# Performance work log

Hardware: AMD Instinct MI355X
Metric: run time of the kernel (lower is better)

Reference implementation:

```python
import jax, jax.numpy as jnp
import numpy as np

B = 1024        # batch of clips
MAX_LEN = 14    # temporal length, pinned by spatial_shapes=[[max_len,1]]
D_MODEL = 1024
N_HEADS = 16
N_POINTS = 4
H_SP, W_SP = MAX_LEN, 1  # level-0 spatial shape (H, W)


def setup_inputs() -> dict:
    key = jax.random.key(0)
    ks = jax.random.split(key, 12)
    s = 0.02
    lin = lambda k, i, o: (jax.random.normal(k, (i, o), jnp.float32) * s)
    vec = lambda k, o: (jax.random.normal(k, (o,), jnp.float32) * s)
    return {
        "x": jax.random.normal(ks[0], (B, MAX_LEN, D_MODEL), jnp.float32),
        "W_value": lin(ks[1], D_MODEL, D_MODEL), "b_value": vec(ks[2], D_MODEL),
        "W_off": lin(ks[3], D_MODEL, N_HEADS * N_POINTS * 2), "b_off": vec(ks[4], N_HEADS * N_POINTS * 2),
        "W_attn": lin(ks[5], D_MODEL, N_HEADS * N_POINTS), "b_attn": vec(ks[6], N_HEADS * N_POINTS),
        "W_out": lin(ks[7], D_MODEL, D_MODEL), "b_out": vec(ks[8], D_MODEL),
        "W_proj": lin(ks[9], D_MODEL, D_MODEL), "b_proj": vec(ks[10], D_MODEL),
    }


def _msdeform(x, W_value, b_value, W_off, b_off, W_attn, b_attn, W_out, b_out):
    Bq, T, D = x.shape
    heads, P = N_HEADS, N_POINTS
    hd = D // heads
    # value projection -> [B, heads, N=H*W, hd]
    value = (x @ W_value + b_value).reshape(Bq, T, heads, hd).transpose(0, 2, 1, 3)
    # sampling offsets [B,T,heads,P,2] and softmax attention weights [B,T,heads,P]
    off = (x @ W_off + b_off).reshape(Bq, T, heads, P, 2)
    aw = jax.nn.softmax((x @ W_attn + b_attn).reshape(Bq, T, heads, P), axis=-1)
    # reference points: x-coord = linspace(0,1,T), y-coord = 0
    ref = jnp.linspace(0.0, 1.0, T, dtype=x.dtype)
    ref_pts = jnp.stack([ref, jnp.zeros_like(ref)], axis=-1)  # [T,2]
    norm = jnp.array([W_SP, H_SP], dtype=x.dtype)  # offset_normalizer = (W, H)
    locs = ref_pts[None, :, None, None, :] + off / norm  # [B,T,heads,P,2] in [0,1] coords
    # grid_sample bilinear, align_corners=False, padding_mode='zeros':
    # pixel coord = loc * size - 0.5
    ix = locs[..., 0] * W_SP - 0.5
    iy = locs[..., 1] * H_SP - 0.5
    x0 = jnp.floor(ix); y0 = jnp.floor(iy)
    fx = ix - x0; fy = iy - y0
    x0i = x0.astype(jnp.int32); y0i = y0.astype(jnp.int32)
    out = jnp.zeros((Bq, heads, T * P, hd), x.dtype)
    corners = ((0, 0, (1 - fx) * (1 - fy)), (1, 0, fx * (1 - fy)),
               (0, 1, (1 - fx) * fy), (1, 1, fx * fy))
    for dx, dy, w in corners:
        xx = x0i + dx; yy = y0i + dy
        valid = ((xx >= 0) & (xx < W_SP) & (yy >= 0) & (yy < H_SP)).astype(x.dtype)
        idx = jnp.clip(yy, 0, H_SP - 1) * W_SP + jnp.clip(xx, 0, W_SP - 1)  # [B,T,heads,P]
        idx_t = idx.transpose(0, 2, 1, 3).reshape(Bq, heads, T * P)
        v = jnp.take_along_axis(value, idx_t[..., None], axis=2)  # [B,heads,T*P,hd]
        wt = (w * valid).transpose(0, 2, 1, 3).reshape(Bq, heads, T * P)
        out = out + v * wt[..., None]
    out = out.reshape(Bq, heads, T, P, hd)
    attn = jnp.einsum('bhqpd,bqhp->bqhd', out, aw).reshape(Bq, T, D)
    return attn @ W_out + b_out


def reference(x, W_value, b_value, W_off, b_off, W_attn, b_attn, W_out, b_out, W_proj, b_proj):
    y = _msdeform(x, W_value, b_value, W_off, b_off, W_attn, b_attn, W_out, b_out)
    return y @ W_proj + b_proj
```

## Files before the change

kernel.cpp:

```cpp
#include <hip/hip_runtime.h>
#include <hip/hip_bf16.h>

using bf16 = __hip_bfloat16;
typedef __attribute__((ext_vector_type(8))) short bf16x8;
typedef __attribute__((ext_vector_type(4))) float f32x4;

#define NB   1024
#define TT   14
#define DM   1024
#define ROWS (NB*TT)
#define NCAT 1280

__device__ __forceinline__ unsigned short f2b(float f) {
  union { bf16 h; unsigned short u; } cv; cv.h = __float2bfloat16(f); return cv.u;
}

__device__ __forceinline__ void gload16(const bf16* g, bf16* l) {
  __builtin_amdgcn_global_load_lds((const __attribute__((address_space(1))) void*)g,
                                   (__attribute__((address_space(3))) void*)l, 16, 0, 0);
}

__global__ __launch_bounds__(256) void k_prep_all(
    const float* __restrict__ x_in,
    const float* __restrict__ Wv, const float* __restrict__ Wo,
    const float* __restrict__ Wa, const float* __restrict__ Wproj,
    const float* __restrict__ Wout,
    const float* __restrict__ bv, const float* __restrict__ bo,
    const float* __restrict__ ba, const float* __restrict__ b_out,
    const float* __restrict__ b_proj,
    bf16* __restrict__ x_bf,
    bf16* __restrict__ wcat_t, bf16* __restrict__ wproj_t,
    bf16* __restrict__ wout_b, float* __restrict__ bcat,
    float* __restrict__ bcomb) {
  __shared__ float t[32][33];
  const int x = blockIdx.x, y = blockIdx.y;
  const int lx = threadIdx.x & 31, ly = threadIdx.x >> 5;
  if (y < 72) {
    const float* src; bf16* dst; int base, width;
    if (y < 40) {
      dst = wcat_t;
      int n0 = y * 32;
      if (n0 < 1024)      { src = Wv; base = 0;    width = 1024; }
      else if (n0 < 1152) { src = Wo; base = 1024; width = 128;  }
      else if (n0 < 1216) { src = Wa; base = 1152; width = 64;   }
      else                { src = nullptr; base = 0; width = 1;  }
      int k0 = x * 32, n0b = n0;
#pragma unroll
      for (int r = 0; r < 32; r += 8)
        t[ly + r][lx] = src ? src[(size_t)(k0 + ly + r) * width + (n0b - base + lx)] : 0.0f;
      __syncthreads();
#pragma unroll
      for (int r = 0; r < 32; r += 8)
        dst[(size_t)(n0b + ly + r) * 1024 + (k0 + lx)] = __float2bfloat16(t[lx][ly + r]);
    } else {
      int n0 = (y - 40) * 32, k0 = x * 32;
#pragma unroll
      for (int r = 0; r < 32; r += 8)
        t[ly + r][lx] = Wproj[(size_t)(k0 + ly + r) * 1024 + (n0 + lx)];
      __syncthreads();
#pragma unroll
      for (int r = 0; r < 32; r += 8)
        wproj_t[(size_t)(n0 + ly + r) * 1024 + (k0 + lx)] = __float2bfloat16(t[lx][ly + r]);
    }
  } else if (y < 80) {
    int i0 = ((y - 72) * 32 + x) * 1024 + threadIdx.x;
#pragma unroll
    for (int r = 0; r < 4; ++r) {
      int i = i0 + r * 256;
      float4 v = reinterpret_cast<const float4*>(Wout)[i];
      ushort4 o;
      o.x = f2b(v.x); o.y = f2b(v.y); o.z = f2b(v.z); o.w = f2b(v.w);
      reinterpret_cast<ushort4*>(wout_b)[i] = o;
    }
  } else if (y == 80) {
    if (x < 5) {
      int i = x * 256 + threadIdx.x;
      if (i < NCAT) {
        float v = 0.0f;
        if (i < 1024) v = bv[i];
        else if (i < 1152) v = bo[i - 1024];
        else if (i < 1216) v = ba[i - 1152];
        bcat[i] = v;
      }
    } else if (x < 21) {
      __shared__ float part[4][64];
      int j0 = (x - 5) * 64;
      int jl = threadIdx.x & 63, ip = threadIdx.x >> 6;
      int j = j0 + jl;
      float acc = 0.0f;
      int i0 = ip * 256;
      for (int i = i0; i < i0 + 256; ++i)
        acc = fmaf(b_out[i], Wproj[(size_t)i * 1024 + j], acc);
      part[ip][jl] = acc;
      __syncthreads();
      if (threadIdx.x < 64) {
        int jj = j0 + threadIdx.x;
        bcomb[jj] = part[0][threadIdx.x] + part[1][threadIdx.x] +
                    part[2][threadIdx.x] + part[3][threadIdx.x] + b_proj[jj];
      }
    }
  } else {
    int id = (y - 81) * 32 + x;
    int i0 = id * 2048 + threadIdx.x;
#pragma unroll
    for (int r = 0; r < 8; ++r) {
      int i = i0 + r * 256;
      float4 v = reinterpret_cast<const float4*>(x_in)[i];
      ushort4 o;
      o.x = f2b(v.x); o.y = f2b(v.y); o.z = f2b(v.z); o.w = f2b(v.w);
      reinterpret_cast<ushort4*>(x_bf)[i] = o;
    }
  }
}

template<int OUT1, int OUT2>
__global__ __launch_bounds__(512, 4) void k_gemm2(
    const bf16* __restrict__ A1, const bf16* __restrict__ B1,
    void* __restrict__ C1v, const float* __restrict__ bias1,
    int N1, int K1, int lda1, int ldb1, int nx1, int nwg1,
    const bf16* __restrict__ A2, const bf16* __restrict__ B2,
    void* __restrict__ C2v, const float* __restrict__ bias2,
    int N2, int K2, int lda2, int ldb2, int nx2) {
  __shared__ bf16 As[3 * 8192];
  __shared__ bf16 Bs[3 * 4096];

  const int tid = threadIdx.x, w = tid >> 6, l = tid & 63;
  const int wm = w >> 1, wn = w & 1;

  const bf16 *A, *Bt; void* Cv; const float* bias;
  int N, K, lda, ldb, bx, by; bool ob;
  if ((int)blockIdx.x < nwg1) {
    int bid = blockIdx.x;
    int q = nwg1 >> 3, r = nwg1 & 7;
    int xcd = bid & 7, li = bid >> 3;
    bid = (xcd < r ? xcd * (q + 1) : r * (q + 1) + (xcd - r) * q) + li;
    A = A1; Bt = B1; Cv = C1v; bias = bias1;
    N = N1; K = K1; lda = lda1; ldb = ldb1;
    bx = bid % nx1; by = bid / nx1; ob = (OUT1 != 0);
  } else {
    int bid = blockIdx.x - nwg1;
    A = A2; Bt = B2; Cv = C2v; bias = bias2;
    N = N2; K = K2; lda = lda2; ldb = ldb2;
    bx = bid % nx2; by = bid / nx2; ob = (OUT2 != 0);
  }
  const int row0 = by * 256, col0 = bx * 128;
  f32x4 acc[4][4] = {};

  const int sr = tid >> 2;
  const int sc = ((tid & 3) ^ (sr & 3)) * 8;
  const bf16* Ab0 = A  + (size_t)(row0 + sr) * lda + sc;
  const bf16* Ab1 = Ab0 + (size_t)128 * lda;
  const bf16* Bb  = Bt + (size_t)(col0 + sr) * ldb + sc;

  const int fr = l & 15, g = l >> 4;
  const int fs = (g ^ (fr & 3)) * 8;
  int aoff[4], boff[4];
#pragma unroll
  for (int i = 0; i < 4; ++i) {
    aoff[i] = (wm * 64 + i * 16 + fr) * 32 + fs;
    boff[i] = (wn * 64 + i * 16 + fr) * 32 + fs;
  }

  auto STAGE = [&](int s, int kt) {
    const int ko = kt * 32;
    gload16(Ab0 + ko, As + s * 8192 + tid * 8);
    gload16(Ab1 + ko, As + s * 8192 + 4096 + tid * 8);
    gload16(Bb  + ko, Bs + s * 4096 + tid * 8);
  };
  auto COMPUTE = [&](int s) {
    const bf16* as = As + s * 8192;
    const bf16* bs = Bs + s * 4096;
    bf16x8 af[4], bfm[4];
#pragma unroll
    for (int i = 0; i < 4; ++i) af[i]  = *(const bf16x8*)(as + aoff[i]);
#pragma unroll
    for (int i = 0; i < 4; ++i) bfm[i] = *(const bf16x8*)(bs + boff[i]);
    __builtin_amdgcn_s_setprio(1);
#pragma unroll
    for (int mi = 0; mi < 4; ++mi)
#pragma unroll
      for (int ni = 0; ni < 4; ++ni)
        acc[mi][ni] = __builtin_amdgcn_mfma_f32_16x16x32_bf16(bfm[ni], af[mi], acc[mi][ni], 0, 0, 0);
    __builtin_amdgcn_s_setprio(0);
  };

  const int nk = K >> 5;
  STAGE(0, 0);
  STAGE(1, 1);
  int cur = 0;
  for (int t = 0; t < nk; ++t) {
    if (t < nk - 1) asm volatile("s_waitcnt vmcnt(3)" ::: "memory");
    else            asm volatile("s_waitcnt vmcnt(0)" ::: "memory");
    __builtin_amdgcn_s_barrier();
    asm volatile("" ::: "memory");
    if (t + 2 < nk) {
      int s2 = cur + 2; if (s2 >= 3) s2 -= 3;
      STAGE(s2, t + 2);
    }
    COMPUTE(cur);
    if (++cur == 3) cur = 0;
  }

#pragma unroll
  for (int mi = 0; mi < 4; ++mi) {
    int gr = row0 + wm * 64 + mi * 16 + fr;
#pragma unroll
    for (int ni = 0; ni < 4; ++ni) {
      int gc = col0 + wn * 64 + ni * 16 + g * 4;
      float b0 = 0, b1 = 0, b2 = 0, b3 = 0;
      if (bias) {
        float4 bv = *reinterpret_cast<const float4*>(bias + gc);
        b0 = bv.x; b1 = bv.y; b2 = bv.z; b3 = bv.w;
      }
      float v0 = acc[mi][ni][0] + b0, v1 = acc[mi][ni][1] + b1;
      float v2 = acc[mi][ni][2] + b2, v3 = acc[mi][ni][3] + b3;
      if (ob) {
        ushort4 u; u.x = f2b(v0); u.y = f2b(v1); u.z = f2b(v2); u.w = f2b(v3);
        *reinterpret_cast<ushort4*>((bf16*)Cv + (size_t)gr * N + gc) = u;
      } else {
        float4 o; o.x = v0; o.y = v1; o.z = v2; o.w = v3;
        *reinterpret_cast<float4*>((float*)Cv + (size_t)gr * N + gc) = o;
      }
    }
  }
}

__global__ __launch_bounds__(256) void k_sample(const bf16* __restrict__ C1,
                                                bf16* __restrict__ y) {
  const int wave = threadIdx.x >> 6, lane = threadIdx.x & 63;
  const int row = blockIdx.x * 4 + wave;
  const int b = row / TT, t = row - b * TT;
  const bf16* r1 = C1 + (size_t)row * NCAT;

  float offx, offy;
  {
    ushort2 u = *reinterpret_cast<const ushort2*>(r1 + 1024 + lane * 2);
    offx = __uint_as_float(((unsigned)u.x) << 16);
    offy = __uint_as_float(((unsigned)u.y) << 16);
  }
  float logit;
  {
    unsigned short u = reinterpret_cast<const unsigned short*>(r1)[1152 + lane];
    logit = __uint_as_float(((unsigned)u) << 16);
  }
  float m = fmaxf(logit, __shfl_xor(logit, 1));
  m = fmaxf(m, __shfl_xor(m, 2));
  float e = __expf(logit - m);
  float s = e + __shfl_xor(e, 1);
  s = s + __shfl_xor(s, 2);
  float aw = e / s;

  const float refx = (float)t * (1.0f / 13.0f);
  float ix = refx + offx - 0.5f;
  float xf = floorf(ix);
  float fx = ix - xf;
  float wx = (xf == 0.0f) ? (1.0f - fx) : ((xf == -1.0f) ? fx : 0.0f);

  float iy = offy - 0.5f;
  float yf = floorf(iy);
  float fy = iy - yf;
  int y0 = (int)yf, y1 = y0 + 1;
  float w0 = (y0 >= 0 && y0 < TT) ? (1.0f - fy) : 0.0f;
  float w1 = (y1 >= 0 && y1 < TT) ? fy : 0.0f;
  int i0 = max(0, min(TT - 1, y0));
  int i1 = max(0, min(TT - 1, y1));
  float cw0 = aw * wx * w0;
  float cw1 = aw * wx * w1;

  const bf16* vb = C1 + (size_t)(b * TT) * NCAT;
  float acc[16];
#pragma unroll
  for (int h = 0; h < 16; ++h) acc[h] = 0.0f;
#pragma unroll
  for (int j = 0; j < 64; ++j) {
    float c0 = __shfl(cw0, j);
    float c1 = __shfl(cw1, j);
    int a0 = __shfl(i0, j);
    int a1 = __shfl(i1, j);
    const int hh = j >> 2;
    float v0 = __bfloat162float(vb[(size_t)a0 * NCAT + hh * 64 + lane]);
    float v1 = __bfloat162float(vb[(size_t)a1 * NCAT + hh * 64 + lane]);
    acc[hh] = fmaf(c0, v0, fmaf(c1, v1, acc[hh]));
  }
#pragma unroll
  for (int h = 0; h < 16; ++h)
    y[(size_t)row * DM + h * 64 + lane] = __float2bfloat16(acc[h]);
}

extern "C" void kernel_launch(void* const* d_in, const int* in_sizes, int n_in,
                              void* d_out, int out_size, void* d_ws, size_t ws_size,
                              hipStream_t stream) {
  (void)in_sizes; (void)n_in; (void)out_size; (void)ws_size;
  const float* x       = (const float*)d_in[0];
  const float* W_value = (const float*)d_in[1];
  const float* b_value = (const float*)d_in[2];
  const float* W_off   = (const float*)d_in[3];
  const float* b_off   = (const float*)d_in[4];
  const float* W_attn  = (const float*)d_in[5];
  const float* b_attn  = (const float*)d_in[6];
  const float* W_out   = (const float*)d_in[7];
  const float* b_out   = (const float*)d_in[8];
  const float* W_proj  = (const float*)d_in[9];
  const float* b_proj  = (const float*)d_in[10];

  char* ws = (char*)d_ws;
  bf16*  x_bf    = (bf16*)(ws);
  bf16*  y_bf    = x_bf;
  bf16*  C1      = (bf16*)(ws + 29360128);
  bf16*  Wcat_t  = (bf16*)(ws + 66060288);
  float* bcat    = (float*)(ws + 68681728);
  bf16*  Wout_b  = (bf16*)(ws + 68686848);
  bf16*  Wproj_t = (bf16*)(ws + 70784000);
  bf16*  Wc_t    = (bf16*)(ws + 72881152);
  float* bcomb   = (float*)(ws + 74978304);

  k_prep_all<<<dim3(32, 137), 256, 0, stream>>>(
      x, W_value, W_off, W_attn, W_proj, W_out,
      b_value, b_off, b_attn, b_out, b_proj,
      x_bf, Wcat_t, Wproj_t, Wout_b, bcat, bcomb);

  k_gemm2<1, 1><<<560 + 32, 512, 0, stream>>>(
      x_bf, Wcat_t, C1, bcat, NCAT, DM, DM, DM, NCAT / 128, 560,
      Wproj_t, Wout_b, Wc_t, nullptr, 1024, 1024, 1024, 1024, 8);

  k_sample<<<ROWS / 4, 256, 0, stream>>>(C1, y_bf);

  k_gemm2<0, 0><<<448, 512, 0, stream>>>(
      y_bf, Wc_t, (float*)d_out, bcomb, DM, DM, DM, DM, DM / 128, 448,
      y_bf, Wc_t, (float*)d_out, bcomb, DM, DM, DM, DM, DM / 128);
}
```

Measured before the change: 176.6 us.

## Switch GEMMs to 256x256 tiles with 8-phase double-buffered K=64 pipeline

Replaces the 256x128-tile, 3-stage GEMM with a 256x256 tile per workgroup. Each of the 8 waves now computes 128x64, and the K step is 64, split into four half-phases that interleave LDS fragment reads, asynchronous global-to-LDS staging and barriers. Larger tiles raise arithmetic intensity and reduce operand reloads. The trade-off is half as many workgroups (296 and 224 on 256 CUs), occupancy of one block per CU, more barriers per K step, and removal of the LDS XOR swizzle, which may cause bank conflicts.

Result: slower. 188.8 us (+6.9%).

```diff
diff --git a/kernel.cpp b/kernel.cpp
--- a/kernel.cpp
+++ b/kernel.cpp
@@ -114,18 +114,17 @@
 }
 
 template<int OUT1, int OUT2>
-__global__ __launch_bounds__(512, 4) void k_gemm2(
+__global__ __launch_bounds__(512, 1) void k_gemm8p(
     const bf16* __restrict__ A1, const bf16* __restrict__ B1,
     void* __restrict__ C1v, const float* __restrict__ bias1,
     int N1, int K1, int lda1, int ldb1, int nx1, int nwg1,
     const bf16* __restrict__ A2, const bf16* __restrict__ B2,
     void* __restrict__ C2v, const float* __restrict__ bias2,
     int N2, int K2, int lda2, int ldb2, int nx2) {
-  __shared__ bf16 As[3 * 8192];
-  __shared__ bf16 Bs[3 * 4096];
-
+  __shared__ bf16 As[2][2][8192];
+  __shared__ bf16 Bs[2][2][8192];
   const int tid = threadIdx.x, w = tid >> 6, l = tid & 63;
-  const int wm = w >> 1, wn = w & 1;
+  const int wm = w >> 2, wn = w & 3;
 
   const bf16 *A, *Bt; void* Cv; const float* bias;
   int N, K, lda, ldb, bx, by; bool ob;
@@ -143,67 +142,67 @@
     N = N2; K = K2; lda = lda2; ldb = ldb2;
     bx = bid % nx2; by = bid / nx2; ob = (OUT2 != 0);
   }
-  const int row0 = by * 256, col0 = bx * 128;
-  f32x4 acc[4][4] = {};
-
-  const int sr = tid >> 2;
-  const int sc = ((tid & 3) ^ (sr & 3)) * 8;
-  const bf16* Ab0 = A  + (size_t)(row0 + sr) * lda + sc;
-  const bf16* Ab1 = Ab0 + (size_t)128 * lda;
-  const bf16* Bb  = Bt + (size_t)(col0 + sr) * ldb + sc;
+  const int row0 = by * 256, col0 = bx * 256;
+
+  const int srow = tid >> 2, sslot = (tid & 3) * 8;
+  const bf16* Ag = A  + (size_t)(row0 + srow) * lda + sslot;
+  const bf16* Bg = Bt + (size_t)(col0 + srow) * ldb + sslot;
+
+#define SA(dd, kh, t) { const int ko = (t) * 64 + (kh) * 32;                    \
+    gload16(Ag + ko,                     &As[dd][kh][srow * 32 + sslot]);       \
+    gload16(Ag + (size_t)128 * lda + ko, &As[dd][kh][(128 + srow) * 32 + sslot]); }
+#define SB(dd, kh, t) { const int ko = (t) * 64 + (kh) * 32;                    \
+    gload16(Bg + ko,                     &Bs[dd][kh][srow * 32 + sslot]);       \
+    gload16(Bg + (size_t)128 * ldb + ko, &Bs[dd][kh][(128 + srow) * 32 + sslot]); }
 
   const int fr = l & 15, g = l >> 4;
-  const int fs = (g ^ (fr & 3)) * 8;
-  int aoff[4], boff[4];
-#pragma unroll
-  for (int i = 0; i < 4; ++i) {
-    aoff[i] = (wm * 64 + i * 16 + fr) * 32 + fs;
-    boff[i] = (wn * 64 + i * 16 + fr) * 32 + fs;
-  }
-
-  auto STAGE = [&](int s, int kt) {
-    const int ko = kt * 32;
-    gload16(Ab0 + ko, As + s * 8192 + tid * 8);
-    gload16(Ab1 + ko, As + s * 8192 + 4096 + tid * 8);
-    gload16(Bb  + ko, Bs + s * 4096 + tid * 8);
-  };
-  auto COMPUTE = [&](int s) {
-    const bf16* as = As + s * 8192;
-    const bf16* bs = Bs + s * 4096;
-    bf16x8 af[4], bfm[4];
-#pragma unroll
-    for (int i = 0; i < 4; ++i) af[i]  = *(const bf16x8*)(as + aoff[i]);
-#pragma unroll
-    for (int i = 0; i < 4; ++i) bfm[i] = *(const bf16x8*)(bs + boff[i]);
-    __builtin_amdgcn_s_setprio(1);
-#pragma unroll
-    for (int mi = 0; mi < 4; ++mi)
-#pragma unroll
-      for (int ni = 0; ni < 4; ++ni)
-        acc[mi][ni] = __builtin_amdgcn_mfma_f32_16x16x32_bf16(bfm[ni], af[mi], acc[mi][ni], 0, 0, 0);
-    __builtin_amdgcn_s_setprio(0);
-  };
-
-  const int nk = K >> 5;
-  STAGE(0, 0);
-  STAGE(1, 1);
-  int cur = 0;
-  for (int t = 0; t < nk; ++t) {
-    if (t < nk - 1) asm volatile("s_waitcnt vmcnt(3)" ::: "memory");
-    else            asm volatile("s_waitcnt vmcnt(0)" ::: "memory");
-    __builtin_amdgcn_s_barrier();
-    asm volatile("" ::: "memory");
-    if (t + 2 < nk) {
-      int s2 = cur + 2; if (s2 >= 3) s2 -= 3;
-      STAGE(s2, t + 2);
-    }
-    COMPUTE(cur);
-    if (++cur == 3) cur = 0;
-  }
-
-#pragma unroll
-  for (int mi = 0; mi < 4; ++mi) {
-    int gr = row0 + wm * 64 + mi * 16 + fr;
+  f32x4 acc[8][4] = {};
+
+  const int nt = K >> 6;
+  SB(0, 0, 0) SA(0, 0, 0) SB(0, 1, 0) SA(0, 1, 0)
+  if (nt > 1) { SB(1, 0, 1) SA(1, 0, 1) SB(1, 1, 1) }
+  asm volatile("s_waitcnt vmcnt(10)" ::: "memory");
+  __builtin_amdgcn_s_barrier();
+  asm volatile("" ::: "memory");
+
+  for (int t = 0; t < nt; ++t) {
+    const int d = t & 1;
+    bf16x8 bfm[4];
+
+#define PH(kh, fh, STAGE_STMT, VMWAIT_STMT)                                      \
+    {                                                                            \
+      bf16x8 af[4];                                                              \
+      _Pragma("unroll") for (int i = 0; i < 4; ++i)                              \
+        af[i] = *(const bf16x8*)&As[d][kh][(wm * 128 + (fh) * 64 + i * 16 + fr) * 32 + g * 8]; \
+      if ((fh) == 0) {                                                           \
+        _Pragma("unroll") for (int i = 0; i < 4; ++i)                            \
+          bfm[i] = *(const bf16x8*)&Bs[d][kh][(wn * 64 + i * 16 + fr) * 32 + g * 8]; \
+      }                                                                          \
+      STAGE_STMT;                                                                \
+      VMWAIT_STMT;                                                               \
+      __builtin_amdgcn_s_barrier();                                              \
+      __builtin_amdgcn_s_setprio(1);                                             \
+      _Pragma("unroll") for (int i = 0; i < 4; ++i)                              \
+        _Pragma("unroll") for (int n = 0; n < 4; ++n)                            \
+          acc[(fh) * 4 + i][n] = __builtin_amdgcn_mfma_f32_16x16x32_bf16(        \
+              bfm[n], af[i], acc[(fh) * 4 + i][n], 0, 0, 0);                     \
+      __builtin_amdgcn_s_setprio(0);                                             \
+      __builtin_amdgcn_s_barrier();                                              \
+      asm volatile("" ::: "memory");                                             \
+    }
+
+    PH(0, 0, { if (t + 1 < nt) SA(d ^ 1, 1, t + 1) }, { })
+    PH(0, 1, { if (t + 2 < nt) SB(d, 0, t + 2) },
+       { if (t < nt - 1) { asm volatile("s_waitcnt vmcnt(4)" ::: "memory"); }
+         else            { asm volatile("s_waitcnt vmcnt(0)" ::: "memory"); } })
+    PH(1, 0, { if (t + 2 < nt) SA(d, 0, t + 2) }, { })
+    PH(1, 1, { if (t + 2 < nt) SB(d, 1, t + 2) }, { })
+#undef PH
+  }
+
+#pragma unroll
+  for (int mi = 0; mi < 8; ++mi) {
+    int gr = row0 + wm * 128 + (mi >> 2) * 64 + (mi & 3) * 16 + fr;
 #pragma unroll
     for (int ni = 0; ni < 4; ++ni) {
       int gc = col0 + wn * 64 + ni * 16 + g * 4;
@@ -223,6 +222,8 @@
       }
     }
   }
+#undef SA
+#undef SB
 }
 
 __global__ __launch_bounds__(256) void k_sample(const bf16* __restrict__ C1,
@@ -319,13 +320,13 @@
       b_value, b_off, b_attn, b_out, b_proj,
       x_bf, Wcat_t, Wproj_t, Wout_b, bcat, bcomb);
 
-  k_gemm2<1, 1><<<560 + 32, 512, 0, stream>>>(
-      x_bf, Wcat_t, C1, bcat, NCAT, DM, DM, DM, NCAT / 128, 560,
-      Wproj_t, Wout_b, Wc_t, nullptr, 1024, 1024, 1024, 1024, 8);
+  k_gemm8p<1, 1><<<280 + 16, 512, 0, stream>>>(
+      x_bf, Wcat_t, C1, bcat, NCAT, DM, DM, DM, 5, 280,
+      Wproj_t, Wout_b, Wc_t, nullptr, 1024, 1024, 1024, 1024, 4);
 
   k_sample<<<ROWS / 4, 256, 0, stream>>>(C1, y_bf);
 
-  k_gemm2<0, 0><<<448, 512, 0, stream>>>(
-      y_bf, Wc_t, (float*)d_out, bcomb, DM, DM, DM, DM, DM / 128, 448,
-      y_bf, Wc_t, (float*)d_out, bcomb, DM, DM, DM, DM, DM / 128);
-}
+  k_gemm8p<0, 0><<<224, 512, 0, stream>>>(
+      y_bf, Wc_t, (float*)d_out, bcomb, DM, DM, DM, DM, 4, 224,
+      y_bf, Wc_t, (float*)d_out, bcomb, DM, DM, DM, DM, 4);
+}
```
